# Kernel optimization log

Hardware: AMD Instinct MI355X
Metric: run time of the kernel (lower is better)

## Reference

```python
import jax, jax.numpy as jnp
import numpy as np

D_MODEL = 1024
BATCH = 4
SEQ = 4096

def setup_inputs() -> dict:
    key = jax.random.key(0)
    k1, k2, k3, k4 = jax.random.split(key, 4)
    scale = 1.0 / np.sqrt(D_MODEL)
    return {
        "inp_emb": jax.random.normal(k1, (BATCH, SEQ, D_MODEL), dtype=jnp.float32),
        "Wq": jax.random.normal(k2, (D_MODEL, D_MODEL), dtype=jnp.float32) * scale,
        "Wk": jax.random.normal(k3, (D_MODEL, D_MODEL), dtype=jnp.float32) * scale,
        "Wv": jax.random.normal(k4, (D_MODEL, D_MODEL), dtype=jnp.float32) * scale,
    }

def reference(inp_emb, Wq, Wk, Wv):
    d_model = Wq.shape[0]
    # torch Linear (no bias): y = x @ W.T
    Q = jnp.einsum('bsd,ed->bse', inp_emb, Wq)
    K = jnp.einsum('bsd,ed->bse', inp_emb, Wk)
    V = jnp.einsum('bsd,ed->bse', inp_emb, Wv)
    scores = jnp.einsum('bqd,bkd->bqk', Q, K) / jnp.sqrt(jnp.float32(d_model))
    probs = jax.nn.softmax(scores, axis=2)
    return jnp.einsum('bqk,bkd->bqd', probs, V)
```

## Files before the change

### kernel.cpp

```cpp
#include <hip/hip_runtime.h>


typedef __bf16 bf16_t;
typedef __bf16 bf16x8 __attribute__((ext_vector_type(8)));
typedef float f32x4 __attribute__((ext_vector_type(4)));

typedef __attribute__((address_space(3))) void lds_void_t;
typedef __attribute__((address_space(1))) void gbl_void_t;

#define SEQ 4096
#define DM  1024

__global__ __launch_bounds__(256) void cast_f32_to_bf16(
    const float* __restrict__ in, bf16_t* __restrict__ out, int n8)
{
    int idx = blockIdx.x * 256 + threadIdx.x;
    if (idx >= n8) return;
    long i = (long)idx * 8;
    f32x4 a = *(const f32x4*)(in + i);
    f32x4 b = *(const f32x4*)(in + i + 4);
    bf16x8 o;
    o[0] = (bf16_t)a[0]; o[1] = (bf16_t)a[1]; o[2] = (bf16_t)a[2]; o[3] = (bf16_t)a[3];
    o[4] = (bf16_t)b[0]; o[5] = (bf16_t)b[1]; o[6] = (bf16_t)b[2]; o[7] = (bf16_t)b[3];
    *(bf16x8*)(out + i) = o;
}

__global__ __launch_bounds__(256) void zero_f32(float* __restrict__ p, int n)
{
    int idx = blockIdx.x * 256 + threadIdx.x;
    if (idx < n) p[idx] = 0.f;
}

template <typename TOUT, int MODE>
__global__ __launch_bounds__(256, 4) void gemm_bt(
    const bf16_t* __restrict__ A, int lda, long sAz,
    const bf16_t* __restrict__ B, int ldb, long sBz,
    TOUT* __restrict__ C, int ldc, long sCz,
    int K, float scale, float* __restrict__ l, long sLz)
{
    __shared__ bf16_t As[128 * 32];
    __shared__ bf16_t Bs[128 * 32];

    A += (long)blockIdx.z * sAz;
    B += (long)blockIdx.z * sBz;
    C += (long)blockIdx.z * sCz;

    const int tid  = threadIdx.x;
    const int wave = tid >> 6;
    const int lane = tid & 63;
    const int m0 = blockIdx.x * 128;
    const int n0 = blockIdx.y * 128;
    const int wm = (wave >> 1) * 64;
    const int wn = (wave & 1) * 64;
    const int mrow = lane & 15;
    const int koff = (lane >> 4) * 8;

    f32x4 acc[4][4];
#pragma unroll
    for (int i = 0; i < 4; ++i)
#pragma unroll
        for (int j = 0; j < 4; ++j)
            acc[i][j] = (f32x4){0.f, 0.f, 0.f, 0.f};

    const int c0 = wave * 2;

    for (int k0 = 0; k0 < K; k0 += 32) {
#pragma unroll
        for (int t = 0; t < 2; ++t) {
            const int chunk = c0 + t;
            const int flat  = chunk * 64 + lane;
            const int row   = flat >> 2;
            const int kp    = (flat & 3) * 8;
            const bf16_t* ga = A + (long)(m0 + row) * lda + (k0 + kp);
            const bf16_t* gb = B + (long)(n0 + row) * ldb + (k0 + kp);
            __builtin_amdgcn_global_load_lds((const gbl_void_t*)ga,
                                             (lds_void_t*)(As + chunk * 512), 16, 0, 0);
            __builtin_amdgcn_global_load_lds((const gbl_void_t*)gb,
                                             (lds_void_t*)(Bs + chunk * 512), 16, 0, 0);
        }
        __syncthreads();

        bf16x8 af[4], bfr[4];
#pragma unroll
        for (int i = 0; i < 4; ++i)
            af[i] = *(const bf16x8*)(As + (wm + i * 16 + mrow) * 32 + koff);
#pragma unroll
        for (int j = 0; j < 4; ++j)
            bfr[j] = *(const bf16x8*)(Bs + (wn + j * 16 + mrow) * 32 + koff);
#pragma unroll
        for (int i = 0; i < 4; ++i)
#pragma unroll
            for (int j = 0; j < 4; ++j)
                acc[i][j] = __builtin_amdgcn_mfma_f32_16x16x32_bf16(af[i], bfr[j], acc[i][j], 0, 0, 0);
        __syncthreads();
    }

    const int col = lane & 15;
    const int r0  = (lane >> 4) * 4;

    if (MODE == 1) {
#pragma unroll
        for (int i = 0; i < 4; ++i)
#pragma unroll
            for (int r = 0; r < 4; ++r) {
                float s = 0.f;
#pragma unroll
                for (int j = 0; j < 4; ++j) {
                    float e = __expf(acc[i][j][r] * scale);
                    acc[i][j][r] = e;
                    s += e;
                }
                s += __shfl_xor(s, 1);
                s += __shfl_xor(s, 2);
                s += __shfl_xor(s, 4);
                s += __shfl_xor(s, 8);
                if (col == 0)
                    atomicAdd(&l[(long)blockIdx.z * sLz + m0 + wm + i * 16 + r0 + r], s);
            }
#pragma unroll
        for (int i = 0; i < 4; ++i)
#pragma unroll
            for (int j = 0; j < 4; ++j)
#pragma unroll
                for (int r = 0; r < 4; ++r)
                    C[(long)(m0 + wm + i * 16 + r0 + r) * ldc + (n0 + wn + j * 16 + col)] =
                        (TOUT)acc[i][j][r];
    } else if (MODE == 2) {
        float inv[4][4];
#pragma unroll
        for (int i = 0; i < 4; ++i)
#pragma unroll
            for (int r = 0; r < 4; ++r)
                inv[i][r] = scale / l[(long)blockIdx.z * sLz + m0 + wm + i * 16 + r0 + r];
#pragma unroll
        for (int i = 0; i < 4; ++i)
#pragma unroll
            for (int j = 0; j < 4; ++j)
#pragma unroll
                for (int r = 0; r < 4; ++r)
                    C[(long)(m0 + wm + i * 16 + r0 + r) * ldc + (n0 + wn + j * 16 + col)] =
                        (TOUT)(acc[i][j][r] * inv[i][r]);
    } else {
#pragma unroll
        for (int i = 0; i < 4; ++i)
#pragma unroll
            for (int j = 0; j < 4; ++j)
#pragma unroll
                for (int r = 0; r < 4; ++r)
                    C[(long)(m0 + wm + i * 16 + r0 + r) * ldc + (n0 + wn + j * 16 + col)] =
                        (TOUT)(acc[i][j][r] * scale);
    }
}

__device__ __forceinline__ float waveMax(float v)
{
#pragma unroll
    for (int o = 32; o > 0; o >>= 1) v = fmaxf(v, __shfl_xor(v, o));
    return v;
}
__device__ __forceinline__ float waveSum(float v)
{
#pragma unroll
    for (int o = 32; o > 0; o >>= 1) v += __shfl_xor(v, o);
    return v;
}

__global__ __launch_bounds__(256) void softmax_rows(bf16_t* __restrict__ S)
{
    const long row = blockIdx.x;
    bf16_t* p = S + row * SEQ;
    const int tid = threadIdx.x;

    float v[16];
    bf16x8 a0 = *(const bf16x8*)(p + tid * 16);
    bf16x8 a1 = *(const bf16x8*)(p + tid * 16 + 8);
#pragma unroll
    for (int i = 0; i < 8; ++i) { v[i] = (float)a0[i]; v[8 + i] = (float)a1[i]; }

    float m = -1e30f;
#pragma unroll
    for (int i = 0; i < 16; ++i) m = fmaxf(m, v[i]);

    __shared__ float redm[4];
    __shared__ float reds[4];
    m = waveMax(m);
    if ((tid & 63) == 0) redm[tid >> 6] = m;
    __syncthreads();
    m = fmaxf(fmaxf(redm[0], redm[1]), fmaxf(redm[2], redm[3]));

    float s = 0.f;
#pragma unroll
    for (int i = 0; i < 16; ++i) { v[i] = __expf(v[i] - m); s += v[i]; }
    s = waveSum(s);
    if ((tid & 63) == 0) reds[tid >> 6] = s;
    __syncthreads();
    s = reds[0] + reds[1] + reds[2] + reds[3];
    const float inv = 1.0f / s;

    bf16x8 o0, o1;
#pragma unroll
    for (int i = 0; i < 8; ++i) {
        o0[i] = (bf16_t)(v[i] * inv);
        o1[i] = (bf16_t)(v[8 + i] * inv);
    }
    *(bf16x8*)(p + tid * 16)     = o0;
    *(bf16x8*)(p + tid * 16 + 8) = o1;
}

__global__ __launch_bounds__(256) void transpose_bf16(
    const bf16_t* __restrict__ in, int ldin, long sInZ,
    bf16_t* __restrict__ out, int ldout, long sOutZ)
{
    in  += (long)blockIdx.z * sInZ;
    out += (long)blockIdx.z * sOutZ;
    __shared__ bf16_t t[32][33];
    const int tx = threadIdx.x;
    const int ty = threadIdx.y;
    const int x  = blockIdx.x * 32 + tx;
    const int y0 = blockIdx.y * 32;
#pragma unroll
    for (int i = 0; i < 4; ++i)
        t[ty + i * 8][tx] = in[(long)(y0 + ty + i * 8) * ldin + x];
    __syncthreads();
    const int xo = blockIdx.x * 32;
#pragma unroll
    for (int i = 0; i < 4; ++i)
        out[(long)(xo + ty + i * 8) * ldout + y0 + tx] = t[tx][ty + i * 8];
}

extern "C" void kernel_launch(void* const* d_in, const int* in_sizes, int n_in,
                              void* d_out, int out_size, void* d_ws, size_t ws_size,
                              hipStream_t stream)
{
    const float* X  = (const float*)d_in[0];
    const float* Wq = (const float*)d_in[1];
    const float* Wk = (const float*)d_in[2];
    const float* Wv = (const float*)d_in[3];
    float* out = (float*)d_out;
    char* ws = (char*)d_ws;

    if (ws_size >= (256ull << 20)) {
        bf16_t* Sbuf = (bf16_t*)ws;
        bf16_t* Xbf  = (bf16_t*)ws;
        bf16_t* Wall = (bf16_t*)(ws + (32l << 20));
        bf16_t* Qbf  = (bf16_t*)(ws + (128l << 20));
        bf16_t* Kbf  = (bf16_t*)(ws + (160l << 20));
        bf16_t* Vbf  = (bf16_t*)(ws + (192l << 20));
        float*  lbuf = (float*)(ws + (192l << 20));
        bf16_t* VT   = (bf16_t*)(ws + (224l << 20));

        cast_f32_to_bf16<<<(16777216 / 8) / 256, 256, 0, stream>>>(X, Xbf, 16777216 / 8);
        cast_f32_to_bf16<<<(1048576 / 8) / 256, 256, 0, stream>>>(Wq, Wall, 1048576 / 8);
        cast_f32_to_bf16<<<(1048576 / 8) / 256, 256, 0, stream>>>(Wk, Wall + 1048576, 1048576 / 8);
        cast_f32_to_bf16<<<(1048576 / 8) / 256, 256, 0, stream>>>(Wv, Wall + 2097152, 1048576 / 8);

        gemm_bt<bf16_t, 0><<<dim3(128, 8, 1), 256, 0, stream>>>(
            Xbf, DM, 0l, Wall, DM, 0l, Qbf, DM, 0l, DM, 1.0f, nullptr, 0l);
        gemm_bt<bf16_t, 0><<<dim3(128, 8, 1), 256, 0, stream>>>(
            Xbf, DM, 0l, Wall + 1048576, DM, 0l, Kbf, DM, 0l, DM, 1.0f, nullptr, 0l);
        gemm_bt<bf16_t, 0><<<dim3(128, 8, 1), 256, 0, stream>>>(
            Xbf, DM, 0l, Wall + 2097152, DM, 0l, Vbf, DM, 0l, DM, 1.0f, nullptr, 0l);

        transpose_bf16<<<dim3(DM / 32, SEQ / 32, 4), dim3(32, 8), 0, stream>>>(
            Vbf, DM, (long)SEQ * DM, VT, SEQ, (long)DM * SEQ);

        zero_f32<<<64, 256, 0, stream>>>(lbuf, 4 * SEQ);

        gemm_bt<bf16_t, 1><<<dim3(32, 32, 4), 256, 0, stream>>>(
            Qbf, DM, (long)SEQ * DM,
            Kbf, DM, (long)SEQ * DM,
            Sbuf, SEQ, (long)SEQ * SEQ, DM, 0.03125f, lbuf, SEQ);

        gemm_bt<float, 2><<<dim3(32, 8, 4), 256, 0, stream>>>(
            Sbuf, SEQ, (long)SEQ * SEQ,
            VT, SEQ, (long)DM * SEQ,
            out, DM, (long)SEQ * DM, SEQ, 1.0f, lbuf, SEQ);
    } else {
        bf16_t* Sbuf = (bf16_t*)ws;
        bf16_t* Xbf  = (bf16_t*)ws;
        bf16_t* Wall = (bf16_t*)(ws + (33l << 20));
        bf16_t* QKV  = (bf16_t*)(ws + (40l << 20));
        bf16_t* VT   = (bf16_t*)(ws + (137l << 20));

        cast_f32_to_bf16<<<(16777216 / 8) / 256, 256, 0, stream>>>(X, Xbf, 16777216 / 8);
        cast_f32_to_bf16<<<(1048576 / 8) / 256, 256, 0, stream>>>(Wq, Wall, 1048576 / 8);
        cast_f32_to_bf16<<<(1048576 / 8) / 256, 256, 0, stream>>>(Wk, Wall + 1048576, 1048576 / 8);
        cast_f32_to_bf16<<<(1048576 / 8) / 256, 256, 0, stream>>>(Wv, Wall + 2097152, 1048576 / 8);

        gemm_bt<bf16_t, 0><<<dim3(128, 24, 1), 256, 0, stream>>>(
            Xbf, DM, 0l, Wall, DM, 0l, QKV, 3072, 0l, DM, 1.0f, nullptr, 0l);

        for (int b = 0; b < 4; ++b) {
            const bf16_t* Qb = QKV + (long)b * SEQ * 3072;
            gemm_bt<bf16_t, 0><<<dim3(32, 32, 1), 256, 0, stream>>>(
                Qb, 3072, 0l, Qb + 1024, 3072, 0l, Sbuf, SEQ, 0l, DM, 0.03125f, nullptr, 0l);
            softmax_rows<<<SEQ, 256, 0, stream>>>(Sbuf);
            transpose_bf16<<<dim3(DM / 32, SEQ / 32, 1), dim3(32, 8), 0, stream>>>(
                Qb + 2048, 3072, 0l, VT, SEQ, 0l);
            gemm_bt<float, 0><<<dim3(32, 8, 1), 256, 0, stream>>>(
                Sbuf, SEQ, 0l, VT, SEQ, 0l, out + (long)b * SEQ * DM, DM, 0l, SEQ, 1.0f, nullptr, 0l);
        }
    }
}
```

Measured before the change: 613.4 us.

## Fold Wq and Wk into a single M matrix to skip Q and K projections

Rewrites the scores as (X·(Wqᵀ·Wk))·Xᵀ. A small 1024×1024 product M = Wkᵀ·Wq is computed once, then T = X·Mᵀ, and the score GEMM runs on T against X directly. This replaces two large projection GEMMs with one large GEMM plus a small one, and also fuses the three weight casts into one launch. The cost is extra bf16 rounding of the composed matrix M, which may change accuracy slightly, plus reshuffled workspace offsets.

```diff
diff --git a/kernel.cpp b/kernel.cpp
--- a/kernel.cpp
+++ b/kernel.cpp
@@ -23,6 +23,20 @@
     o[0] = (bf16_t)a[0]; o[1] = (bf16_t)a[1]; o[2] = (bf16_t)a[2]; o[3] = (bf16_t)a[3];
     o[4] = (bf16_t)b[0]; o[5] = (bf16_t)b[1]; o[6] = (bf16_t)b[2]; o[7] = (bf16_t)b[3];
     *(bf16x8*)(out + i) = o;
+}
+
+__global__ __launch_bounds__(256) void cast3_w(
+    const float* __restrict__ w0, const float* __restrict__ w1,
+    const float* __restrict__ w2, bf16_t* __restrict__ out)
+{
+    const float* in = (blockIdx.z == 0) ? w0 : (blockIdx.z == 1) ? w1 : w2;
+    long i = ((long)blockIdx.x * 256 + threadIdx.x) * 8;
+    f32x4 a = *(const f32x4*)(in + i);
+    f32x4 b = *(const f32x4*)(in + i + 4);
+    bf16x8 o;
+    o[0] = (bf16_t)a[0]; o[1] = (bf16_t)a[1]; o[2] = (bf16_t)a[2]; o[3] = (bf16_t)a[3];
+    o[4] = (bf16_t)b[0]; o[5] = (bf16_t)b[1]; o[6] = (bf16_t)b[2]; o[7] = (bf16_t)b[3];
+    *(bf16x8*)(out + (long)blockIdx.z * 1048576 + i) = o;
 }
 
 __global__ __launch_bounds__(256) void zero_f32(float* __restrict__ p, int n)
@@ -240,35 +254,40 @@
     char* ws = (char*)d_ws;
 
     if (ws_size >= (256ull << 20)) {
-        bf16_t* Sbuf = (bf16_t*)ws;
         bf16_t* Xbf  = (bf16_t*)ws;
-        bf16_t* Wall = (bf16_t*)(ws + (32l << 20));
-        bf16_t* Qbf  = (bf16_t*)(ws + (128l << 20));
-        bf16_t* Kbf  = (bf16_t*)(ws + (160l << 20));
-        bf16_t* Vbf  = (bf16_t*)(ws + (192l << 20));
-        float*  lbuf = (float*)(ws + (192l << 20));
-        bf16_t* VT   = (bf16_t*)(ws + (224l << 20));
+        bf16_t* Vbf  = (bf16_t*)(ws + (32l << 20));
+        bf16_t* Tbuf = (bf16_t*)(ws + (32l << 20));
+        bf16_t* VT   = (bf16_t*)(ws + (64l << 20));
+        bf16_t* Sbuf = (bf16_t*)(ws + (96l << 20));
+        bf16_t* Wall = (bf16_t*)(ws + (224l << 20));
+        bf16_t* WqT  = (bf16_t*)(ws + (230l << 20));
+        bf16_t* WkT  = (bf16_t*)(ws + (232l << 20));
+        bf16_t* Mt   = (bf16_t*)(ws + (234l << 20));
+        float*  lbuf = (float*)(ws + (236l << 20));
 
         cast_f32_to_bf16<<<(16777216 / 8) / 256, 256, 0, stream>>>(X, Xbf, 16777216 / 8);
-        cast_f32_to_bf16<<<(1048576 / 8) / 256, 256, 0, stream>>>(Wq, Wall, 1048576 / 8);
-        cast_f32_to_bf16<<<(1048576 / 8) / 256, 256, 0, stream>>>(Wk, Wall + 1048576, 1048576 / 8);
-        cast_f32_to_bf16<<<(1048576 / 8) / 256, 256, 0, stream>>>(Wv, Wall + 2097152, 1048576 / 8);
-
-        gemm_bt<bf16_t, 0><<<dim3(128, 8, 1), 256, 0, stream>>>(
-            Xbf, DM, 0l, Wall, DM, 0l, Qbf, DM, 0l, DM, 1.0f, nullptr, 0l);
-        gemm_bt<bf16_t, 0><<<dim3(128, 8, 1), 256, 0, stream>>>(
-            Xbf, DM, 0l, Wall + 1048576, DM, 0l, Kbf, DM, 0l, DM, 1.0f, nullptr, 0l);
+        cast3_w<<<dim3(512, 1, 3), 256, 0, stream>>>(Wq, Wk, Wv, Wall);
+
+        transpose_bf16<<<dim3(32, 32, 2), dim3(32, 8), 0, stream>>>(
+            Wall, DM, 1048576, WqT, DM, 1048576);
+
+        gemm_bt<bf16_t, 0><<<dim3(8, 8, 1), 256, 0, stream>>>(
+            WkT, DM, 0l, WqT, DM, 0l, Mt, DM, 0l, DM, 1.0f, nullptr, 0l);
+
         gemm_bt<bf16_t, 0><<<dim3(128, 8, 1), 256, 0, stream>>>(
             Xbf, DM, 0l, Wall + 2097152, DM, 0l, Vbf, DM, 0l, DM, 1.0f, nullptr, 0l);
 
         transpose_bf16<<<dim3(DM / 32, SEQ / 32, 4), dim3(32, 8), 0, stream>>>(
             Vbf, DM, (long)SEQ * DM, VT, SEQ, (long)DM * SEQ);
 
+        gemm_bt<bf16_t, 0><<<dim3(128, 8, 1), 256, 0, stream>>>(
+            Xbf, DM, 0l, Mt, DM, 0l, Tbuf, DM, 0l, DM, 1.0f, nullptr, 0l);
+
         zero_f32<<<64, 256, 0, stream>>>(lbuf, 4 * SEQ);
 
         gemm_bt<bf16_t, 1><<<dim3(32, 32, 4), 256, 0, stream>>>(
-            Qbf, DM, (long)SEQ * DM,
-            Kbf, DM, (long)SEQ * DM,
+            Tbuf, DM, (long)SEQ * DM,
+            Xbf, DM, (long)SEQ * DM,
             Sbuf, SEQ, (long)SEQ * SEQ, DM, 0.03125f, lbuf, SEQ);
 
         gemm_bt<float, 2><<<dim3(32, 8, 4), 256, 0, stream>>>(
@@ -283,9 +302,7 @@
         bf16_t* VT   = (bf16_t*)(ws + (137l << 20));
 
         cast_f32_to_bf16<<<(16777216 / 8) / 256, 256, 0, stream>>>(X, Xbf, 16777216 / 8);
-        cast_f32_to_bf16<<<(1048576 / 8) / 256, 256, 0, stream>>>(Wq, Wall, 1048576 / 8);
-        cast_f32_to_bf16<<<(1048576 / 8) / 256, 256, 0, stream>>>(Wk, Wall + 1048576, 1048576 / 8);
-        cast_f32_to_bf16<<<(1048576 / 8) / 256, 256, 0, stream>>>(Wv, Wall + 2097152, 1048576 / 8);
+        cast3_w<<<dim3(512, 1, 3), 256, 0, stream>>>(Wq, Wk, Wv, Wall);
 
         gemm_bt<bf16_t, 0><<<dim3(128, 24, 1), 256, 0, stream>>>(
             Xbf, DM, 0l, Wall, DM, 0l, QKV, 3072, 0l, DM, 1.0f, nullptr, 0l);
```

After: 565.3 us. -7.9%, faster.
